# Kernel tuning notes

Measured on AMD Instinct MI355X. Metric: run time of the kernel, lower is better.

The kernel has to match this reference:

```python
import jax, jax.numpy as jnp
import numpy as np

N = 8192
C = 256


def setup_inputs() -> dict:
    key = jax.random.key(0)
    k_x, k_wr, k_br, k_wc, k_bc = jax.random.split(key, 5)
    scale = 1.0 / np.sqrt(C)
    return {
        "x": jax.random.normal(k_x, (N, C), dtype=jnp.float32),
        "w_reduce": jax.random.uniform(k_wr, (C, C), dtype=jnp.float32, minval=-scale, maxval=scale),
        "b_reduce": jax.random.uniform(k_br, (C,), dtype=jnp.float32, minval=-scale, maxval=scale),
        "w_contr": jax.random.uniform(k_wc, (1, C), dtype=jnp.float32, minval=-scale, maxval=scale),
        "b_contr": jax.random.uniform(k_bc, (1,), dtype=jnp.float32, minval=-scale, maxval=scale),
    }


def reference(x, w_reduce, b_reduce, w_contr, b_contr):
    # Original math: y_ij = reduce(x_i + x_j); z_ij = sigmoid(contr(y_ij));
    # out_i = mean_j y_ij * z_ij.
    # Since reduce/contr are affine, decompose without the [N,N,C] tensor:
    #   y_ij = r_i + r_j + b_reduce,        r = x @ Wr^T
    #   contr(y_ij) = s_i + s_j + c0,       s = r . wc, c0 = b_reduce . wc + bc
    n = x.shape[0]
    r = x @ w_reduce.T                                   # [N, C]
    wc = w_contr[0]                                      # [C]
    s = r @ wc                                           # [N]
    c0 = b_reduce @ wc + b_contr[0]                      # scalar
    Z = jax.nn.sigmoid(s[:, None] + s[None, :] + c0)     # [N, N] pairwise gate
    m = jnp.mean(Z, axis=1, keepdims=True)               # [N, 1]
    # mean_j (r_i + r_j + b) * z_ij = (r_i + b) * m_i + (Z @ r)_i / N
    out = (r + b_reduce) * m + (Z @ r) / n               # [N, C]
    return out
```

## Files before the change

kernel.cpp:

```cpp
#include <hip/hip_runtime.h>
#include <hip/hip_bf16.h>
#include <stdint.h>

#define NN 8192
#define CC 256
#define NSPLIT 8
#define JR (NN / NSPLIT)
#define NITER (JR / 32)

typedef float f32x4 __attribute__((ext_vector_type(4)));
typedef float f32x2 __attribute__((ext_vector_type(2)));
typedef short s16x8 __attribute__((ext_vector_type(8)));

#define LOG2E 1.4426950408889634f

#define OFF_WT  0
#define OFF_R   (OFF_WT + CC*CC)
#define OFF_S2  (OFF_R + NN*CC)
#define OFF_C0  (OFF_S2 + NN)
#define OFF_SS  (OFF_C0 + 16)
#define OFF_SP  (OFF_SS + NSPLIT*NN)
#define OFF_V   (OFF_SP + 4*NN)
#define OFF_RB  (OFF_V + (NSPLIT*NN*CC)/2)

__global__ __launch_bounds__(256) void k_prep(const float* __restrict__ w,
                                              const float* __restrict__ br,
                                              const float* __restrict__ wcv,
                                              const float* __restrict__ bc,
                                              float* __restrict__ ws) {
  int k = blockIdx.x, c = threadIdx.x;
  ws[OFF_WT + k * CC + c] = w[c * CC + k];
  if (blockIdx.x == 0 && threadIdx.x < 64) {
    int lane = threadIdx.x;
    f32x4 b4 = *(const f32x4*)&br[lane * 4];
    f32x4 w4 = *(const f32x4*)&wcv[lane * 4];
    float d = b4[0]*w4[0] + b4[1]*w4[1] + b4[2]*w4[2] + b4[3]*w4[3];
    #pragma unroll
    for (int m = 32; m >= 1; m >>= 1) d += __shfl_xor(d, m, 64);
    if (lane == 0) { ws[OFF_C0] = d + bc[0]; ws[OFF_C0 + 1] = (d + bc[0]) * LOG2E; }
  }
}

__global__ __launch_bounds__(256) void k_r(const float* __restrict__ x,
                                           const float* __restrict__ wcv,
                                           float* __restrict__ ws) {
  __shared__ float xs[64][260];
  int bi = blockIdx.x;
  int rowblk = bi >> 2, colblk = bi & 3;
  int tid = threadIdx.x;
  int i0 = rowblk * 64;
  for (int t = tid; t < 64 * 64; t += 256) {
    int rr = t >> 6, c4 = t & 63;
    *(f32x4*)&xs[rr][c4 * 4] = *(const f32x4*)&x[(i0 + rr) * CC + c4 * 4];
  }
  __syncthreads();
  int tx = tid & 15, ty = tid >> 4;
  int cbase = colblk * 64 + tx * 4;
  int r0 = ty * 4;
  float acc[4][4] = {};
  const float* wt = ws + OFF_WT;
  for (int k = 0; k < CC; k += 2) {
    f32x4 wv0 = *(const f32x4*)&wt[k * CC + cbase];
    f32x4 wv1 = *(const f32x4*)&wt[(k + 1) * CC + cbase];
    f32x2 xv[4];
    #pragma unroll
    for (int rr = 0; rr < 4; rr++) xv[rr] = *(const f32x2*)&xs[r0 + rr][k];
    #pragma unroll
    for (int rr = 0; rr < 4; rr++)
      #pragma unroll
      for (int cc = 0; cc < 4; cc++)
        acc[rr][cc] = fmaf(xv[rr][1], wv1[cc], fmaf(xv[rr][0], wv0[cc], acc[rr][cc]));
  }
  #pragma unroll
  for (int rr = 0; rr < 4; rr++) {
    f32x4 o = {acc[rr][0], acc[rr][1], acc[rr][2], acc[rr][3]};
    *(f32x4*)&ws[OFF_R + (size_t)(i0 + r0 + rr) * CC + cbase] = o;
  }
  unsigned* rb32 = (unsigned*)(ws + OFF_RB);
  int j0r = i0 + r0;
  #pragma unroll
  for (int cc = 0; cc < 4; cc++) {
    int c = cbase + cc;
    unsigned pk = 0;
    pk = __builtin_amdgcn_cvt_pk_fp8_f32(acc[0][cc], acc[1][cc], (int)pk, false);
    pk = __builtin_amdgcn_cvt_pk_fp8_f32(acc[2][cc], acc[3][cc], (int)pk, true);
    int us = (((j0r >> 5) * 16 + (c >> 4)) * 64 + (((j0r >> 3) & 3) * 16 + (c & 15))) * 8 + (j0r & 7);
    rb32[us >> 2] = pk;
  }
  f32x4 wc4 = *(const f32x4*)&wcv[cbase];
  float sd[4];
  #pragma unroll
  for (int rr = 0; rr < 4; rr++) {
    sd[rr] = acc[rr][0]*wc4[0] + acc[rr][1]*wc4[1] + acc[rr][2]*wc4[2] + acc[rr][3]*wc4[3];
    #pragma unroll
    for (int m = 1; m < 16; m <<= 1) sd[rr] += __shfl_xor(sd[rr], m, 64);
  }
  if (tx == 0) {
    #pragma unroll
    for (int rr = 0; rr < 4; rr++)
      ws[OFF_SP + colblk * NN + j0r + rr] = sd[rr];
  }
}

__global__ __launch_bounds__(256) void k_s2(float* __restrict__ ws) {
  int row = blockIdx.x * 256 + threadIdx.x;
  float s = ws[OFF_SP + row] + ws[OFF_SP + NN + row]
          + ws[OFF_SP + 2 * NN + row] + ws[OFF_SP + 3 * NN + row];
  ws[OFF_S2 + row] = s * LOG2E;
}


#define STAGE(BUF, IT) { \
  const char* gb_ = rbase + (size_t)(IT) * 8192 + w * 1024 + l * 16; \
  _Pragma("unroll") \
  for (int q_ = 0; q_ < 2; q_++) \
    __builtin_amdgcn_global_load_lds( \
      (const __attribute__((address_space(1))) void*)(gb_ + q_ * 4096), \
      (__attribute__((address_space(3))) void*)&ldsb[(BUF) * 8192 + w * 1024 + q_ * 4096], \
      16, 0, 0); }

#define WAITBAR2 { asm volatile("s_waitcnt vmcnt(2)" ::: "memory"); \
  __builtin_amdgcn_s_barrier(); \
  __builtin_amdgcn_sched_barrier(0); }

#define WAITBAR0 { asm volatile("s_waitcnt vmcnt(0)" ::: "memory"); \
  __builtin_amdgcn_s_barrier(); \
  __builtin_amdgcn_sched_barrier(0); }

#define SB0 __builtin_amdgcn_sched_barrier(0);

#define SIGMOID(IT, AFA, AFB) { \
  f32x4 sj0_ = *(const f32x4*)&s2l[(IT) * 32 + g * 8]; \
  f32x4 sj1_ = *(const f32x4*)&s2l[(IT) * 32 + g * 8 + 4]; \
  float zA_[8], zB_[8]; \
  _Pragma("unroll") \
  for (int t_ = 0; t_ < 8; t_++) { \
    float sj_ = (t_ < 4) ? sj0_[t_] : sj1_[t_ - 4]; \
    float eA_, eB_; \
    asm("v_exp_f32 %0, %1" : "=v"(eA_) : "v"(negaA - sj_)); \
    asm("v_exp_f32 %0, %1" : "=v"(eB_) : "v"(negaB - sj_)); \
    zA_[t_] = __builtin_amdgcn_rcpf(1.0f + eA_); \
    zB_[t_] = __builtin_amdgcn_rcpf(1.0f + eB_); } \
  unsigned loA_ = 0, hiA_ = 0, loB_ = 0, hiB_ = 0; \
  loA_ = __builtin_amdgcn_cvt_pk_fp8_f32(zA_[0], zA_[1], (int)loA_, false); \
  loA_ = __builtin_amdgcn_cvt_pk_fp8_f32(zA_[2], zA_[3], (int)loA_, true); \
  hiA_ = __builtin_amdgcn_cvt_pk_fp8_f32(zA_[4], zA_[5], (int)hiA_, false); \
  hiA_ = __builtin_amdgcn_cvt_pk_fp8_f32(zA_[6], zA_[7], (int)hiA_, true); \
  loB_ = __builtin_amdgcn_cvt_pk_fp8_f32(zB_[0], zB_[1], (int)loB_, false); \
  loB_ = __builtin_amdgcn_cvt_pk_fp8_f32(zB_[2], zB_[3], (int)loB_, true); \
  hiB_ = __builtin_amdgcn_cvt_pk_fp8_f32(zB_[4], zB_[5], (int)hiB_, false); \
  hiB_ = __builtin_amdgcn_cvt_pk_fp8_f32(zB_[6], zB_[7], (int)hiB_, true); \
  AFA = (long)(((unsigned long long)hiA_ << 32) | loA_); \
  AFB = (long)(((unsigned long long)hiB_ << 32) | loB_); }

#define BLOAD(BF, LP) { \
  _Pragma("unroll") \
  for (int ct_ = 0; ct_ < 16; ct_++) \
    BF[ct_] = *(const long*)((LP) + ct_ * 512 + l * 8); }

#define MFMA_APPLY(AFA, AFB, BF) { \
  _Pragma("unroll") \
  for (int ct_ = 0; ct_ < 16; ct_++) { \
    accA[ct_] = __builtin_amdgcn_mfma_f32_16x16x32_fp8_fp8(AFA, BF[ct_], accA[ct_], 0, 0, 0); \
    accB[ct_] = __builtin_amdgcn_mfma_f32_16x16x32_fp8_fp8(AFB, BF[ct_], accB[ct_], 0, 0, 0); } \
  acc1A = __builtin_amdgcn_mfma_f32_16x16x32_fp8_fp8(AFA, ones, acc1A, 0, 0, 0); \
  acc1B = __builtin_amdgcn_mfma_f32_16x16x32_fp8_fp8(AFB, ones, acc1B, 0, 0, 0); }

__global__ __launch_bounds__(256, 2) void k_main(float* __restrict__ ws) {
  __shared__ char ldsb[3 * 8192];
  __shared__ float s2l[1024];
  int blk = blockIdx.x;
  int rt = blk >> 3, h = blk & 7;
  int tid = threadIdx.x;
  int w = tid >> 6, l = tid & 63;
  int lr = l & 15, g = l >> 4;
  int iw = rt * 128 + w * 32;
  float c02 = ws[OFF_C0 + 1];
  float negaA = -(ws[OFF_S2 + iw + lr] + c02);
  float negaB = -(ws[OFF_S2 + iw + 16 + lr] + c02);

  const float* s2p = ws + OFF_S2 + h * JR;
  *(f32x4*)&s2l[tid * 4] = *(const f32x4*)(s2p + tid * 4);
  __syncthreads();

  f32x4 accA[16], accB[16], acc1A, acc1B;
  #pragma unroll
  for (int i = 0; i < 16; i++) { accA[i] = (f32x4)(0.f); accB[i] = (f32x4)(0.f); }
  acc1A = (f32x4)(0.f); acc1B = (f32x4)(0.f);
  const long ones = 0x3838383838383838LL;

  const char* rbase = (const char*)(ws + OFF_RB) + (size_t)h * (JR * CC);

  STAGE(0, 0);
  STAGE(1, 1);
  long afA0, afB0, afA1, afB1;
  long bf[16];
  SIGMOID(0, afA0, afB0);

  int sA = 0;
  #pragma unroll 1
  for (int J = 0; J < NITER - 2; J += 2) {
    int sB = sA + 1; if (sB == 3) sB = 0;
    int sC = sB + 1; if (sC == 3) sC = 0;

    WAITBAR2;
    STAGE(sC, J + 2);
    SB0;
    BLOAD(bf, ldsb + sA * 8192);
    SB0;
    SIGMOID(J + 1, afA1, afB1);
    MFMA_APPLY(afA0, afB0, bf);

    WAITBAR2;
    STAGE(sA, J + 3);
    SB0;
    BLOAD(bf, ldsb + sB * 8192);
    SB0;
    SIGMOID(J + 2, afA0, afB0);
    MFMA_APPLY(afA1, afB1, bf);

    sA = sC;
  }
  {
    int sB = sA + 1; if (sB == 3) sB = 0;
    WAITBAR2;
    BLOAD(bf, ldsb + sA * 8192);
    SB0;
    SIGMOID(NITER - 1, afA1, afB1);
    MFMA_APPLY(afA0, afB0, bf);
    WAITBAR0;
    BLOAD(bf, ldsb + sB * 8192);
    MFMA_APPLY(afA1, afB1, bf);
  }

  if (lr == 0) {
    #pragma unroll
    for (int q = 0; q < 4; q++) {
      ws[OFF_SS + h * NN + iw + g * 4 + q] = acc1A[q];
      ws[OFF_SS + h * NN + iw + 16 + g * 4 + q] = acc1B[q];
    }
  }
  unsigned short* Vb = (unsigned short*)(ws + OFF_V);
  size_t vbase = (size_t)h * (NN * CC);
  #pragma unroll
  for (int ct = 0; ct < 16; ct++) {
    #pragma unroll
    for (int q = 0; q < 4; q++) {
      unsigned uA = __float_as_uint(accA[ct][q]);
      uA = (uA + 0x7fffu + ((uA >> 16) & 1u)) >> 16;
      Vb[vbase + (size_t)(iw + g * 4 + q) * CC + ct * 16 + lr] = (unsigned short)uA;
      unsigned uB = __float_as_uint(accB[ct][q]);
      uB = (uB + 0x7fffu + ((uB >> 16) & 1u)) >> 16;
      Vb[vbase + (size_t)(iw + 16 + g * 4 + q) * CC + ct * 16 + lr] = (unsigned short)uB;
    }
  }
}

__global__ __launch_bounds__(256) void k_epi(const float* __restrict__ br,
                                             const float* __restrict__ ws,
                                             float* __restrict__ out) {
  int idx = blockIdx.x * 256 + threadIdx.x;
  int i = idx >> 5, c8 = (idx & 31) * 8;
  float S = 0.f;
  #pragma unroll
  for (int p = 0; p < NSPLIT; p++) S += ws[OFF_SS + p * NN + i];
  float m = S * (1.0f / NN);
  float v[8] = {};
  const unsigned short* Vb = (const unsigned short*)(ws + OFF_V);
  #pragma unroll
  for (int p = 0; p < NSPLIT; p++) {
    s16x8 pv = *(const s16x8*)&Vb[(size_t)p * (NN * CC) + (size_t)i * CC + c8];
    #pragma unroll
    for (int t = 0; t < 8; t++)
      v[t] += __uint_as_float(((unsigned)(unsigned short)pv[t]) << 16);
  }
  f32x4 r0 = *(const f32x4*)&ws[OFF_R + (size_t)i * CC + c8];
  f32x4 r1 = *(const f32x4*)&ws[OFF_R + (size_t)i * CC + c8 + 4];
  f32x4 b0 = *(const f32x4*)&br[c8];
  f32x4 b1 = *(const f32x4*)&br[c8 + 4];
  f32x4 o0, o1;
  #pragma unroll
  for (int t = 0; t < 4; t++) {
    o0[t] = (r0[t] + b0[t]) * m + v[t] * (1.0f / NN);
    o1[t] = (r1[t] + b1[t]) * m + v[t + 4] * (1.0f / NN);
  }
  *(f32x4*)&out[(size_t)i * CC + c8] = o0;
  *(f32x4*)&out[(size_t)i * CC + c8 + 4] = o1;
}

extern "C" void kernel_launch(void* const* d_in, const int* in_sizes, int n_in,
                              void* d_out, int out_size, void* d_ws, size_t ws_size,
                              hipStream_t stream) {
  const float* x  = (const float*)d_in[0];
  const float* w  = (const float*)d_in[1];
  const float* br = (const float*)d_in[2];
  const float* wc = (const float*)d_in[3];
  const float* bc = (const float*)d_in[4];
  float* ws = (float*)d_ws;
  float* out = (float*)d_out;
  (void)in_sizes; (void)n_in; (void)out_size; (void)ws_size;

  k_prep<<<256, 256, 0, stream>>>(w, br, wc, bc, ws);
  k_r<<<512, 256, 0, stream>>>(x, wc, ws);
  k_s2<<<32, 256, 0, stream>>>(ws);
  k_main<<<512, 256, 0, stream>>>(ws);
  k_epi<<<1024, 256, 0, stream>>>(br, ws, out);
}
```

Baseline: 80.20 us.

## Load B fragments directly from global memory, dropping LDS staging and barriers

Removes the triple-buffered LDS staging of the fp8 r operand (global_load_lds plus waitcnt and barriers). Each wave now reads its MFMA B fragments straight from global memory into registers, double-buffered across iterations. The aim is to remove the barrier synchronisation and LDS traffic. In exchange, every wave in a block issues redundant global loads of the same data, and register pressure rises because two 16-element fragment buffers are held at once. The last iteration recomputes a clamped index, which adds an extra redundant load and sigmoid.

```diff
diff --git a/kernel.cpp b/kernel.cpp
--- a/kernel.cpp
+++ b/kernel.cpp
@@ -109,25 +109,6 @@
   ws[OFF_S2 + row] = s * LOG2E;
 }
 
-
-#define STAGE(BUF, IT) { \
-  const char* gb_ = rbase + (size_t)(IT) * 8192 + w * 1024 + l * 16; \
-  _Pragma("unroll") \
-  for (int q_ = 0; q_ < 2; q_++) \
-    __builtin_amdgcn_global_load_lds( \
-      (const __attribute__((address_space(1))) void*)(gb_ + q_ * 4096), \
-      (__attribute__((address_space(3))) void*)&ldsb[(BUF) * 8192 + w * 1024 + q_ * 4096], \
-      16, 0, 0); }
-
-#define WAITBAR2 { asm volatile("s_waitcnt vmcnt(2)" ::: "memory"); \
-  __builtin_amdgcn_s_barrier(); \
-  __builtin_amdgcn_sched_barrier(0); }
-
-#define WAITBAR0 { asm volatile("s_waitcnt vmcnt(0)" ::: "memory"); \
-  __builtin_amdgcn_s_barrier(); \
-  __builtin_amdgcn_sched_barrier(0); }
-
-#define SB0 __builtin_amdgcn_sched_barrier(0);
 
 #define SIGMOID(IT, AFA, AFB) { \
   f32x4 sj0_ = *(const f32x4*)&s2l[(IT) * 32 + g * 8]; \
@@ -153,10 +134,10 @@
   AFA = (long)(((unsigned long long)hiA_ << 32) | loA_); \
   AFB = (long)(((unsigned long long)hiB_ << 32) | loB_); }
 
-#define BLOAD(BF, LP) { \
+#define LOADB(BF, CI) { \
   _Pragma("unroll") \
   for (int ct_ = 0; ct_ < 16; ct_++) \
-    BF[ct_] = *(const long*)((LP) + ct_ * 512 + l * 8); }
+    BF[ct_] = rbs[(((CI) << 4) + ct_) * 64 + l]; }
 
 #define MFMA_APPLY(AFA, AFB, BF) { \
   _Pragma("unroll") \
@@ -167,14 +148,14 @@
   acc1B = __builtin_amdgcn_mfma_f32_16x16x32_fp8_fp8(AFB, ones, acc1B, 0, 0, 0); }
 
 __global__ __launch_bounds__(256, 2) void k_main(float* __restrict__ ws) {
-  __shared__ char ldsb[3 * 8192];
   __shared__ float s2l[1024];
   int blk = blockIdx.x;
   int rt = blk >> 3, h = blk & 7;
   int tid = threadIdx.x;
   int w = tid >> 6, l = tid & 63;
   int lr = l & 15, g = l >> 4;
-  int iw = rt * 128 + w * 32;
+  (void)w;
+  int iw = rt * 128 + (tid >> 6) * 32;
   float c02 = ws[OFF_C0 + 1];
   float negaA = -(ws[OFF_S2 + iw + lr] + c02);
   float negaB = -(ws[OFF_S2 + iw + 16 + lr] + c02);
@@ -189,48 +170,21 @@
   acc1A = (f32x4)(0.f); acc1B = (f32x4)(0.f);
   const long ones = 0x3838383838383838LL;
 
-  const char* rbase = (const char*)(ws + OFF_RB) + (size_t)h * (JR * CC);
-
-  STAGE(0, 0);
-  STAGE(1, 1);
+  const long* rbs = (const long*)((const char*)(ws + OFF_RB) + (size_t)h * (JR * CC));
+
+  long bfA[16], bfB[16];
   long afA0, afB0, afA1, afB1;
-  long bf[16];
+  LOADB(bfA, 0);
   SIGMOID(0, afA0, afB0);
-
-  int sA = 0;
   #pragma unroll 1
-  for (int J = 0; J < NITER - 2; J += 2) {
-    int sB = sA + 1; if (sB == 3) sB = 0;
-    int sC = sB + 1; if (sC == 3) sC = 0;
-
-    WAITBAR2;
-    STAGE(sC, J + 2);
-    SB0;
-    BLOAD(bf, ldsb + sA * 8192);
-    SB0;
+  for (int J = 0; J < NITER; J += 2) {
+    LOADB(bfB, J + 1);
     SIGMOID(J + 1, afA1, afB1);
-    MFMA_APPLY(afA0, afB0, bf);
-
-    WAITBAR2;
-    STAGE(sA, J + 3);
-    SB0;
-    BLOAD(bf, ldsb + sB * 8192);
-    SB0;
-    SIGMOID(J + 2, afA0, afB0);
-    MFMA_APPLY(afA1, afB1, bf);
-
-    sA = sC;
-  }
-  {
-    int sB = sA + 1; if (sB == 3) sB = 0;
-    WAITBAR2;
-    BLOAD(bf, ldsb + sA * 8192);
-    SB0;
-    SIGMOID(NITER - 1, afA1, afB1);
-    MFMA_APPLY(afA0, afB0, bf);
-    WAITBAR0;
-    BLOAD(bf, ldsb + sB * 8192);
-    MFMA_APPLY(afA1, afB1, bf);
+    MFMA_APPLY(afA0, afB0, bfA);
+    int J2 = (J + 2 < NITER) ? J + 2 : J + 1;
+    LOADB(bfA, J2);
+    SIGMOID(J2, afA0, afB0);
+    MFMA_APPLY(afA1, afB1, bfB);
   }
 
   if (lr == 0) {
```

Result: slower. 87.10 us (+8.6%).
